# Performance work log

Hardware: AMD Instinct MI355X
Metric: run time of the kernel (lower is better)

Reference implementation:

```python
import jax, jax.numpy as jnp
import numpy as np

B, N, D, A, H, DFF = 4, 2048, 1024, 1024, 16, 4096
HD = A // H
SCALE = D ** (-0.5)  # module uses d_model**-0.5, not head_dim
EPS = 1e-5


def setup_inputs() -> dict:
    key = jax.random.key(0)
    ks = jax.random.split(key, 16)
    s = lambda k, shp, fan: jax.random.normal(k, shp, jnp.float32) * (fan ** -0.5)
    return {
        "x": jax.random.normal(ks[0], (B, N, D), jnp.float32),
        "mask": jnp.zeros((B, 1, N, N), dtype=bool),
        "wq": s(ks[1], (A, D), D), "bq": jnp.zeros((A,), jnp.float32),
        "wk": s(ks[2], (A, D), D), "bk": jnp.zeros((A,), jnp.float32),
        "wv": s(ks[3], (A, D), D), "bv": jnp.zeros((A,), jnp.float32),
        "wo": s(ks[4], (D, A), A), "bo": jnp.zeros((D,), jnp.float32),
        "w1": s(ks[5], (DFF, D), D), "b1": jnp.zeros((DFF,), jnp.float32),
        "w2": s(ks[6], (D, DFF), DFF), "b2": jnp.zeros((D,), jnp.float32),
        "ln1_g": jnp.ones((D,), jnp.float32), "ln1_b": jnp.zeros((D,), jnp.float32),
        "ln2_g": jnp.ones((D,), jnp.float32), "ln2_b": jnp.zeros((D,), jnp.float32),
    }


def _ln(x, g, b):
    m = x.mean(-1, keepdims=True)
    v = jnp.mean((x - m) ** 2, -1, keepdims=True)
    return (x - m) * jax.lax.rsqrt(v + EPS) * g + b


def reference(x, mask, wq, bq, wk, bk, wv, bv, wo, bo, w1, b1, w2, b2,
              ln1_g, ln1_b, ln2_g, ln2_b):
    # --- pre-norm self attention ---
    h = _ln(x, ln1_g, ln1_b)
    def heads(w, bias):  # (B,N,D) -> (B,H,N,HD)
        y = h @ w.T + bias
        return y.reshape(B, N, H, HD).transpose(0, 2, 1, 3)
    q, k, v = heads(wq, bq), heads(wk, bk), heads(wv, bv)
    scores = jnp.einsum('bhnd,bhmd->bhnm', q, k) * SCALE
    scores = jnp.where(mask, -jnp.inf, scores)
    attn = jax.nn.softmax(scores, axis=-1)  # dropout = identity in eval
    o = jnp.einsum('bhnm,bhmd->bhnd', attn, v)
    o = o.transpose(0, 2, 1, 3).reshape(B, N, A)
    x = (o @ wo.T + bo) + x
    # --- pre-norm MLP ---
    h2 = _ln(x, ln2_g, ln2_b)
    m = jax.nn.relu(h2 @ w1.T + b1) @ w2.T + b2
    return m + x
```

## Files before the change

### kernel.cpp

```cpp
#include <hip/hip_runtime.h>
#include <hip/hip_bf16.h>
#include <stdint.h>

#define Bb 4
#define Nn 2048
#define Dd 1024
#define Aa 1024
#define Hh 16
#define HDd 64
#define DFF 4096
#define Mm (Bb*Nn)

typedef __bf16 bf16x8 __attribute__((ext_vector_type(8)));
typedef float f32x4 __attribute__((ext_vector_type(4)));
typedef float f32x16 __attribute__((ext_vector_type(16)));
typedef uint32_t u32x4v __attribute__((ext_vector_type(4)));
typedef unsigned short ushort_t;
using bf16 = __hip_bfloat16;

#define LOG2E 1.44269504088896340736f

__device__ inline ushort_t f2bfu(float f) {
  uint32_t u = __builtin_bit_cast(uint32_t, f);
  uint32_t r = u + 0x7fffu + ((u >> 16) & 1u);
  return (ushort_t)(r >> 16);
}
__device__ inline uint32_t pk2(float lo, float hi) {
  return ((uint32_t)f2bfu(hi) << 16) | (uint32_t)f2bfu(lo);
}

#define GLOAD_LDS16(gsrc, ldst)                                                \
  __builtin_amdgcn_global_load_lds(                                            \
      (const __attribute__((address_space(1))) void*)(gsrc),                   \
      (__attribute__((address_space(3))) void*)(ldst), 16, 0, 0)

__global__ __launch_bounds__(256) void cvt_k(const float* __restrict__ in,
                                             bf16* __restrict__ out, int n4) {
  int i = blockIdx.x * 256 + threadIdx.x;
  if (i >= n4) return;
  float4 v = reinterpret_cast<const float4*>(in)[i];
  ushort4 o;
  o.x = f2bfu(v.x); o.y = f2bfu(v.y); o.z = f2bfu(v.z); o.w = f2bfu(v.w);
  reinterpret_cast<ushort4*>(out)[i] = o;
}

__global__ __launch_bounds__(256) void ln_k(const float* __restrict__ x,
                                            const float* __restrict__ g,
                                            const float* __restrict__ b,
                                            bf16* __restrict__ out) {
  const int row = blockIdx.x;
  const int t = threadIdx.x;
  const float4 v = reinterpret_cast<const float4*>(x + (size_t)row * Dd)[t];
  float s = v.x + v.y + v.z + v.w;
  float sq = v.x * v.x + v.y * v.y + v.z * v.z + v.w * v.w;
#pragma unroll
  for (int m = 1; m < 64; m <<= 1) {
    s += __shfl_xor(s, m);
    sq += __shfl_xor(sq, m);
  }
  __shared__ float red[8];
  if ((t & 63) == 0) { red[t >> 6] = s; red[4 + (t >> 6)] = sq; }
  __syncthreads();
  s = red[0] + red[1] + red[2] + red[3];
  sq = red[4] + red[5] + red[6] + red[7];
  const float mean = s * (1.f / Dd);
  const float rstd = rsqrtf(sq * (1.f / Dd) - mean * mean + 1e-5f);
  const float4 gg = reinterpret_cast<const float4*>(g)[t];
  const float4 bb = reinterpret_cast<const float4*>(b)[t];
  ushort4 o;
  o.x = f2bfu((v.x - mean) * rstd * gg.x + bb.x);
  o.y = f2bfu((v.y - mean) * rstd * gg.y + bb.y);
  o.z = f2bfu((v.z - mean) * rstd * gg.z + bb.z);
  o.w = f2bfu((v.w - mean) * rstd * gg.w + bb.w);
  reinterpret_cast<ushort4*>(out + (size_t)row * Dd)[t] = o;
}

template <int EPI>
__global__ __launch_bounds__(256) void gemm_bt(const bf16* __restrict__ Amat,
                                               const bf16* __restrict__ Wmat,
                                               const float* __restrict__ bias,
                                               const float* __restrict__ resid,
                                               void* __restrict__ Cout,
                                               int Ndim, int Kdim, float ascale) {
  __shared__ __align__(16) bf16 As[128 * 32];
  __shared__ __align__(16) bf16 Bs[128 * 32];
  const int tid = threadIdx.x;
  const int wave = tid >> 6, lane = tid & 63;
  const int g16 = lane >> 4, l15 = lane & 15;
  const int wm = wave >> 1, wn = wave & 1;
  const int tmb = blockIdx.y * 128, tnb = blockIdx.x * 128;

  const f32x4 zero = {0.f, 0.f, 0.f, 0.f};
  f32x4 acc[4][4];
#pragma unroll
  for (int f = 0; f < 4; f++)
#pragma unroll
    for (int g = 0; g < 4; g++) acc[f][g] = zero;

  for (int k0 = 0; k0 < Kdim; k0 += 32) {
    __syncthreads();
#pragma unroll
    for (int i = 0; i < 2; i++) {
      int c = i * 256 + tid;
      int row = c >> 2, cw = c & 3;
      GLOAD_LDS16(Amat + (size_t)(tmb + row) * Kdim + k0 + cw * 8,
                  As + (i * 256 + wave * 64) * 8);
      GLOAD_LDS16(Wmat + (size_t)(tnb + row) * Kdim + k0 + cw * 8,
                  Bs + (i * 256 + wave * 64) * 8);
    }
    __syncthreads();
    bf16x8 af[4], bfr[4];
#pragma unroll
    for (int f = 0; f < 4; f++) {
      af[f] = *reinterpret_cast<const bf16x8*>(As + (wm * 64 + f * 16 + l15) * 32 + g16 * 8);
      bfr[f] = *reinterpret_cast<const bf16x8*>(Bs + (wn * 64 + f * 16 + l15) * 32 + g16 * 8);
    }
#pragma unroll
    for (int f = 0; f < 4; f++)
#pragma unroll
      for (int g = 0; g < 4; g++)
        acc[f][g] = __builtin_amdgcn_mfma_f32_16x16x32_bf16(af[f], bfr[g], acc[f][g], 0, 0, 0);
  }

#pragma unroll
  for (int f = 0; f < 4; f++) {
#pragma unroll
    for (int g = 0; g < 4; g++) {
      const int col = tnb + wn * 64 + g * 16 + l15;
      const float bi = bias[col];
#pragma unroll
      for (int r = 0; r < 4; r++) {
        const int row = tmb + wm * 64 + f * 16 + g16 * 4 + r;
        float v = (acc[f][g][r] + bi) * ascale;
        if constexpr (EPI == 2) v = fmaxf(v, 0.f);
        if constexpr (EPI == 1) {
          ((float*)Cout)[(size_t)row * Ndim + col] = v + resid[(size_t)row * Ndim + col];
        } else {
          ((bf16*)Cout)[(size_t)row * Ndim + col] = __float2bfloat16(v);
        }
      }
    }
  }
}

__global__ __launch_bounds__(256) void vtrans_k(const bf16* __restrict__ vm,
                                                bf16* __restrict__ vt) {
  const int bh = blockIdx.y, b = bh >> 4, h = bh & 15;
  const int n0 = blockIdx.x * 64;
  __shared__ __align__(16) bf16 tile[64 * 72];
  const int tid = threadIdx.x;
#pragma unroll
  for (int i = 0; i < 2; i++) {
    int c = i * 256 + tid;
    int r = c >> 3, cw = c & 7;
    bf16x8 v = *reinterpret_cast<const bf16x8*>(vm + (size_t)(b * Nn + n0 + r) * Aa + h * HDd + cw * 8);
    *reinterpret_cast<bf16x8*>(tile + r * 72 + cw * 8) = v;
  }
  __syncthreads();
#pragma unroll
  for (int i = 0; i < 2; i++) {
    int c = i * 256 + tid;
    int d = c >> 3, ncw = c & 7;
    alignas(16) bf16 tmp[8];
#pragma unroll
    for (int e = 0; e < 8; e++) tmp[e] = tile[(ncw * 8 + e) * 72 + d];
    *reinterpret_cast<bf16x8*>(vt + (size_t)(bh * HDd + d) * Nn + n0 + ncw * 8) =
        *reinterpret_cast<bf16x8*>(tmp);
  }
}

__global__ __launch_bounds__(256) void attn_k(const bf16* __restrict__ qm,
                                              const bf16* __restrict__ km,
                                              const bf16* __restrict__ vtm,
                                              bf16* __restrict__ om) {
  const int bh = blockIdx.y, b = bh >> 4, h = bh & 15;
  const int tid = threadIdx.x;
  const int wv = tid >> 6, lane = tid & 63;
  const int l31 = lane & 31, hi = lane >> 5, l7 = lane & 7;

  __shared__ __align__(16) bf16 SMEM[16384];

  const int q0 = blockIdx.x * 128 + wv * 32;

  bf16x8 qf[4];
  const size_t qbase = (size_t)(b * Nn + q0 + l31) * Aa + h * HDd + hi * 8;
#pragma unroll
  for (int dk = 0; dk < 4; dk++)
    qf[dk] = *reinterpret_cast<const bf16x8*>(qm + qbase + dk * 16);

  f32x16 oacc[2];
#pragma unroll
  for (int d = 0; d < 2; d++)
#pragma unroll
    for (int r = 0; r < 16; r++) oacc[d][r] = 0.f;
  float mrun = -__builtin_huge_valf(), lrun = 0.f;

#define STAGE(buf, j0)                                                         \
  {                                                                            \
    _Pragma("unroll")                                                          \
    for (int i = 0; i < 2; i++) {                                              \
      int id = i * 256 + tid;                                                  \
      int row = id >> 3, c = id & 7;                                           \
      int cs = c ^ (row & 7);                                                  \
      GLOAD_LDS16(km + (size_t)(b * Nn + (j0) + row) * Aa + h * HDd + cs * 8,  \
                  SMEM + (buf) * 4096 + (i * 256 + wv * 64) * 8);              \
      GLOAD_LDS16(vtm + (size_t)(bh * 64 + row) * Nn + (j0) + cs * 8,          \
                  SMEM + 8192 + (buf) * 4096 + (i * 256 + wv * 64) * 8);       \
    }                                                                          \
  }

  STAGE(0, 0)
  asm volatile("s_waitcnt vmcnt(0)" ::: "memory");
  __builtin_amdgcn_s_barrier();

  const int NT = Nn / 64;
  for (int jt = 0; jt < NT; jt++) {
    const int cur = jt & 1;
    if (jt + 1 < NT) STAGE(cur ^ 1, (jt + 1) * 64)
    const bf16* KBc = SMEM + cur * 4096;
    const bf16* VBc = SMEM + 8192 + cur * 4096;

    f32x16 sacc[2];
#pragma unroll
    for (int t = 0; t < 2; t++)
#pragma unroll
      for (int r = 0; r < 16; r++) sacc[t][r] = 0.f;
#pragma unroll
    for (int t = 0; t < 2; t++) {
#pragma unroll
      for (int dk = 0; dk < 4; dk++) {
        const int row = t * 32 + l31;
        const bf16x8 kf = *reinterpret_cast<const bf16x8*>(
            KBc + row * 64 + (((hi + 2 * dk) ^ l7) * 8));
        sacc[t] = __builtin_amdgcn_mfma_f32_32x32x16_bf16(kf, qf[dk], sacc[t], 0, 0, 0);
      }
    }

    float tm = sacc[0][0];
#pragma unroll
    for (int r = 1; r < 16; r++) tm = fmaxf(tm, sacc[0][r]);
#pragma unroll
    for (int r = 0; r < 16; r++) tm = fmaxf(tm, sacc[1][r]);
    tm = fmaxf(tm, __shfl_xor(tm, 32));
    const float nm = fmaxf(mrun, tm);
    const float corr = exp2f((mrun - nm) * LOG2E);
    mrun = nm;

    float ps = 0.f;
    uint32_t w[8][2];
#pragma unroll
    for (int a = 0; a < 8; a++) {
#pragma unroll
      for (int bb = 0; bb < 2; bb++) {
        const int t = a >> 2, r = (a & 3) * 4 + 2 * bb;
        const float p0 = exp2f((sacc[t][r] - nm) * LOG2E);
        const float p1 = exp2f((sacc[t][r + 1] - nm) * LOG2E);
        ps += p0 + p1;
        w[a][bb] = pk2(p0, p1);
      }
    }
    ps += __shfl_xor(ps, 32);
    lrun = lrun * corr + ps;
#pragma unroll
    for (int d = 0; d < 2; d++)
#pragma unroll
      for (int r = 0; r < 16; r++) oacc[d][r] *= corr;

#pragma unroll
    for (int ks = 0; ks < 4; ks++) {
      const uint32_t wl0 = hi ? w[2 * ks + 1][0] : w[2 * ks][0];
      const uint32_t wl1 = hi ? w[2 * ks + 1][1] : w[2 * ks][1];
      const uint32_t ws0 = hi ? w[2 * ks][0] : w[2 * ks + 1][0];
      const uint32_t ws1 = hi ? w[2 * ks][1] : w[2 * ks + 1][1];
      const uint32_t wr0 = __shfl_xor(ws0, 32);
      const uint32_t wr1 = __shfl_xor(ws1, 32);
      u32x4v w4;
      w4[0] = hi ? wr0 : wl0;
      w4[1] = hi ? wr1 : wl1;
      w4[2] = hi ? wl0 : wr0;
      w4[3] = hi ? wl1 : wr1;
      const bf16x8 pf = __builtin_bit_cast(bf16x8, w4);
#pragma unroll
      for (int dh = 0; dh < 2; dh++) {
        const int row = dh * 32 + l31;
        const bf16x8 vf = *reinterpret_cast<const bf16x8*>(
            VBc + row * 64 + (((hi + 2 * ks) ^ l7) * 8));
        oacc[dh] = __builtin_amdgcn_mfma_f32_32x32x16_bf16(vf, pf, oacc[dh], 0, 0, 0);
      }
    }

    if (jt + 1 < NT) {
      asm volatile("s_waitcnt vmcnt(0)" ::: "memory");
      __builtin_amdgcn_s_barrier();
    }
  }

  __syncthreads();
  bf16* ob = SMEM + wv * (32 * 72);
  const float inv = 1.f / lrun;
#pragma unroll
  for (int dh = 0; dh < 2; dh++) {
#pragma unroll
    for (int r = 0; r < 16; r++) {
      const int d = (r & 3) + 8 * (r >> 2) + 4 * hi + 32 * dh;
      ob[l31 * 72 + d] = __float2bfloat16(oacc[dh][r] * inv);
    }
  }
  __syncthreads();
  const int qp = lane >> 1, half = lane & 1;
  const size_t orow = (size_t)(b * Nn + q0 + qp) * Aa + h * HDd + half * 32;
#pragma unroll
  for (int e = 0; e < 2; e++) {
    bf16x8 v0 = *reinterpret_cast<const bf16x8*>(ob + qp * 72 + half * 32 + e * 16);
    bf16x8 v1 = *reinterpret_cast<const bf16x8*>(ob + qp * 72 + half * 32 + e * 16 + 8);
    *reinterpret_cast<bf16x8*>(om + orow + e * 16) = v0;
    *reinterpret_cast<bf16x8*>(om + orow + e * 16 + 8) = v1;
  }
}

extern "C" void kernel_launch(void* const* d_in, const int* in_sizes, int n_in,
                              void* d_out, int out_size, void* d_ws, size_t ws_size,
                              hipStream_t stream) {
  const float* x    = (const float*)d_in[0];
  const float* wq   = (const float*)d_in[2];
  const float* bq   = (const float*)d_in[3];
  const float* wk   = (const float*)d_in[4];
  const float* bk   = (const float*)d_in[5];
  const float* wv   = (const float*)d_in[6];
  const float* bv   = (const float*)d_in[7];
  const float* wo   = (const float*)d_in[8];
  const float* bo   = (const float*)d_in[9];
  const float* w1   = (const float*)d_in[10];
  const float* b1   = (const float*)d_in[11];
  const float* w2   = (const float*)d_in[12];
  const float* b2   = (const float*)d_in[13];
  const float* ln1g = (const float*)d_in[14];
  const float* ln1b = (const float*)d_in[15];
  const float* ln2g = (const float*)d_in[16];
  const float* ln2b = (const float*)d_in[17];
  float* out = (float*)d_out;

  uint8_t* ws = (uint8_t*)d_ws;
  const size_t MB = (size_t)1 << 20;
  bf16* wq_b = (bf16*)(ws + 0 * MB);
  bf16* wk_b = (bf16*)(ws + 2 * MB);
  bf16* wv_b = (bf16*)(ws + 4 * MB);
  bf16* wo_b = (bf16*)(ws + 6 * MB);
  bf16* w1_b = (bf16*)(ws + 8 * MB);
  bf16* w2_b = (bf16*)(ws + 16 * MB);
  bf16* h_b  = (bf16*)(ws + 24 * MB);
  bf16* q_b  = (bf16*)(ws + 40 * MB);
  bf16* k_b  = (bf16*)(ws + 56 * MB);
  bf16* v_b  = (bf16*)(ws + 72 * MB);
  bf16* vt_b = (bf16*)(ws + 88 * MB);
  bf16* o_b  = (bf16*)(ws + 104 * MB);
  float* x2  = (float*)(ws + 120 * MB);
  bf16* mid  = (bf16*)(ws + 40 * MB);

  const float SCALE = 0.03125f;

  cvt_k<<<1024, 256, 0, stream>>>(wq, wq_b, 262144);
  cvt_k<<<1024, 256, 0, stream>>>(wk, wk_b, 262144);
  cvt_k<<<1024, 256, 0, stream>>>(wv, wv_b, 262144);
  cvt_k<<<1024, 256, 0, stream>>>(wo, wo_b, 262144);
  cvt_k<<<4096, 256, 0, stream>>>(w1, w1_b, 1048576);
  cvt_k<<<4096, 256, 0, stream>>>(w2, w2_b, 1048576);

  ln_k<<<Mm, 256, 0, stream>>>(x, ln1g, ln1b, h_b);

  dim3 gP(Aa / 128, Mm / 128);
  gemm_bt<0><<<gP, 256, 0, stream>>>(h_b, wq_b, bq, nullptr, q_b, Aa, Dd, SCALE);
  gemm_bt<0><<<gP, 256, 0, stream>>>(h_b, wk_b, bk, nullptr, k_b, Aa, Dd, 1.f);
  gemm_bt<0><<<gP, 256, 0, stream>>>(h_b, wv_b, bv, nullptr, v_b, Aa, Dd, 1.f);

  vtrans_k<<<dim3(Nn / 64, Bb * Hh), 256, 0, stream>>>(v_b, vt_b);
  attn_k<<<dim3(Nn / 128, Bb * Hh), 256, 0, stream>>>(q_b, k_b, vt_b, o_b);

  gemm_bt<1><<<gP, 256, 0, stream>>>(o_b, wo_b, bo, x, x2, Dd, Aa, 1.f);

  ln_k<<<Mm, 256, 0, stream>>>(x2, ln2g, ln2b, h_b);

  dim3 gF(DFF / 128, Mm / 128);
  gemm_bt<2><<<gF, 256, 0, stream>>>(h_b, w1_b, b1, nullptr, mid, DFF, Dd, 1.f);
  gemm_bt<1><<<gP, 256, 0, stream>>>(mid, w2_b, b2, x2, out, Dd, DFF, 1.f);
}
```

Baseline: 692.5 us.

## Swizzle GEMM LDS layout, lazy softmax rescale, hardware bf16 pack, permlane swap

The GEMM tiles are now stored in LDS with an XOR-swizzled two-rows-per-64-element layout, so the MFMA fragment reads avoid bank conflicts. The attention kernel skips rescaling the output accumulator unless the running max grows by more than a threshold (lazy rescale). It also packs to bf16 with v_cvt_pk_bf16_f32, replaces the shuffle-based P fragment exchange with v_permlane32_swap, and splits the row-sum into independent partial sums. The attention grid is transposed so that heads vary fastest, which changes K/V cache locality. The lazy rescale lets unnormalized exponentials reach up to 2^(8*log2e) before normalization, which carries a small numeric risk.

After: 659.2 us. -4.8%, faster.

```diff
diff --git a/kernel.cpp b/kernel.cpp
--- a/kernel.cpp
+++ b/kernel.cpp
@@ -24,9 +24,6 @@
   uint32_t u = __builtin_bit_cast(uint32_t, f);
   uint32_t r = u + 0x7fffu + ((u >> 16) & 1u);
   return (ushort_t)(r >> 16);
-}
-__device__ inline uint32_t pk2(float lo, float hi) {
-  return ((uint32_t)f2bfu(hi) << 16) | (uint32_t)f2bfu(lo);
 }
 
 #define GLOAD_LDS16(gsrc, ldst)                                                \
@@ -101,19 +98,26 @@
     __syncthreads();
 #pragma unroll
     for (int i = 0; i < 2; i++) {
-      int c = i * 256 + tid;
-      int row = c >> 2, cw = c & 3;
-      GLOAD_LDS16(Amat + (size_t)(tmb + row) * Kdim + k0 + cw * 8,
+      int t = i * 256 + tid;
+      int lr = t >> 3;
+      int s8 = (t & 7) ^ (lr & 7);
+      int row = lr * 2 + (s8 >> 2);
+      int cs = s8 & 3;
+      GLOAD_LDS16(Amat + (size_t)(tmb + row) * Kdim + k0 + cs * 8,
                   As + (i * 256 + wave * 64) * 8);
-      GLOAD_LDS16(Wmat + (size_t)(tnb + row) * Kdim + k0 + cw * 8,
+      GLOAD_LDS16(Wmat + (size_t)(tnb + row) * Kdim + k0 + cs * 8,
                   Bs + (i * 256 + wave * 64) * 8);
     }
     __syncthreads();
     bf16x8 af[4], bfr[4];
 #pragma unroll
     for (int f = 0; f < 4; f++) {
-      af[f] = *reinterpret_cast<const bf16x8*>(As + (wm * 64 + f * 16 + l15) * 32 + g16 * 8);
-      bfr[f] = *reinterpret_cast<const bf16x8*>(Bs + (wn * 64 + f * 16 + l15) * 32 + g16 * 8);
+      const int rA = wm * 64 + f * 16 + l15;
+      const int rB = wn * 64 + f * 16 + l15;
+      af[f] = *reinterpret_cast<const bf16x8*>(
+          As + (rA >> 1) * 64 + (((((rA & 1) << 2) + g16) ^ ((rA >> 1) & 7)) * 8));
+      bfr[f] = *reinterpret_cast<const bf16x8*>(
+          Bs + (rB >> 1) * 64 + (((((rB & 1) << 2) + g16) ^ ((rB >> 1) & 7)) * 8));
     }
 #pragma unroll
     for (int f = 0; f < 4; f++)
@@ -173,14 +177,14 @@
                                               const bf16* __restrict__ km,
                                               const bf16* __restrict__ vtm,
                                               bf16* __restrict__ om) {
-  const int bh = blockIdx.y, b = bh >> 4, h = bh & 15;
+  const int bh = blockIdx.x, b = bh >> 4, h = bh & 15;
   const int tid = threadIdx.x;
   const int wv = tid >> 6, lane = tid & 63;
   const int l31 = lane & 31, hi = lane >> 5, l7 = lane & 7;
 
   __shared__ __align__(16) bf16 SMEM[16384];
 
-  const int q0 = blockIdx.x * 128 + wv * 32;
+  const int q0 = blockIdx.y * 128 + wv * 32;
 
   bf16x8 qf[4];
   const size_t qbase = (size_t)(b * Nn + q0 + l31) * Aa + h * HDd + hi * 8;
@@ -236,49 +240,52 @@
       }
     }
 
-    float tm = sacc[0][0];
-#pragma unroll
-    for (int r = 1; r < 16; r++) tm = fmaxf(tm, sacc[0][r]);
+    float tm = fmaxf(sacc[0][0], sacc[0][1]);
+#pragma unroll
+    for (int r = 2; r < 16; r++) tm = fmaxf(tm, sacc[0][r]);
 #pragma unroll
     for (int r = 0; r < 16; r++) tm = fmaxf(tm, sacc[1][r]);
     tm = fmaxf(tm, __shfl_xor(tm, 32));
-    const float nm = fmaxf(mrun, tm);
-    const float corr = exp2f((mrun - nm) * LOG2E);
-    mrun = nm;
-
-    float ps = 0.f;
-    uint32_t w[8][2];
-#pragma unroll
-    for (int a = 0; a < 8; a++) {
-#pragma unroll
-      for (int bb = 0; bb < 2; bb++) {
-        const int t = a >> 2, r = (a & 3) * 4 + 2 * bb;
-        const float p0 = exp2f((sacc[t][r] - nm) * LOG2E);
-        const float p1 = exp2f((sacc[t][r + 1] - nm) * LOG2E);
-        ps += p0 + p1;
-        w[a][bb] = pk2(p0, p1);
+
+    if (!__all(tm <= mrun + 8.f)) {
+      const float nmv = fmaxf(mrun, tm);
+      const float corr = exp2f((mrun - nmv) * LOG2E);
+      mrun = nmv;
+      lrun *= corr;
+#pragma unroll
+      for (int d = 0; d < 2; d++)
+#pragma unroll
+        for (int r = 0; r < 16; r++) oacc[d][r] *= corr;
+    }
+    const float nmL = mrun * LOG2E;
+    float ps0 = 0.f, ps1 = 0.f, ps2 = 0.f, ps3 = 0.f;
+    uint32_t Wx[2][8];
+#pragma unroll
+    for (int t = 0; t < 2; t++) {
+#pragma unroll
+      for (int j = 0; j < 8; j++) {
+        const float p0 = exp2f(fmaf(sacc[t][2 * j], LOG2E, -nmL));
+        const float p1 = exp2f(fmaf(sacc[t][2 * j + 1], LOG2E, -nmL));
+        if (j & 2) { if (j & 1) ps3 += p0 + p1; else ps2 += p0 + p1; }
+        else       { if (j & 1) ps1 += p0 + p1; else ps0 += p0 + p1; }
+        uint32_t w;
+        asm("v_cvt_pk_bf16_f32 %0, %1, %2" : "=v"(w) : "v"(p0), "v"(p1));
+        Wx[t][j] = w;
       }
     }
+    float ps = (ps0 + ps1) + (ps2 + ps3);
     ps += __shfl_xor(ps, 32);
-    lrun = lrun * corr + ps;
-#pragma unroll
-    for (int d = 0; d < 2; d++)
-#pragma unroll
-      for (int r = 0; r < 16; r++) oacc[d][r] *= corr;
+    lrun += ps;
 
 #pragma unroll
     for (int ks = 0; ks < 4; ks++) {
-      const uint32_t wl0 = hi ? w[2 * ks + 1][0] : w[2 * ks][0];
-      const uint32_t wl1 = hi ? w[2 * ks + 1][1] : w[2 * ks][1];
-      const uint32_t ws0 = hi ? w[2 * ks][0] : w[2 * ks + 1][0];
-      const uint32_t ws1 = hi ? w[2 * ks][1] : w[2 * ks + 1][1];
-      const uint32_t wr0 = __shfl_xor(ws0, 32);
-      const uint32_t wr1 = __shfl_xor(ws1, 32);
+      const int tt = ks >> 1, bse = (ks & 1) * 4;
+      uint32_t w0 = Wx[tt][bse + 0], w1 = Wx[tt][bse + 1];
+      uint32_t w2 = Wx[tt][bse + 2], w3 = Wx[tt][bse + 3];
+      asm("v_permlane32_swap_b32 %0, %1" : "+v"(w0), "+v"(w2));
+      asm("v_permlane32_swap_b32 %0, %1" : "+v"(w1), "+v"(w3));
       u32x4v w4;
-      w4[0] = hi ? wr0 : wl0;
-      w4[1] = hi ? wr1 : wl1;
-      w4[2] = hi ? wl0 : wr0;
-      w4[3] = hi ? wl1 : wr1;
+      w4[0] = w0; w4[1] = w1; w4[2] = w2; w4[3] = w3;
       const bf16x8 pf = __builtin_bit_cast(bf16x8, w4);
 #pragma unroll
       for (int dh = 0; dh < 2; dh++) {
@@ -374,7 +381,7 @@
   gemm_bt<0><<<gP, 256, 0, stream>>>(h_b, wv_b, bv, nullptr, v_b, Aa, Dd, 1.f);
 
   vtrans_k<<<dim3(Nn / 64, Bb * Hh), 256, 0, stream>>>(v_b, vt_b);
-  attn_k<<<dim3(Nn / 128, Bb * Hh), 256, 0, stream>>>(q_b, k_b, vt_b, o_b);
+  attn_k<<<dim3(Bb * Hh, Nn / 128), 256, 0, stream>>>(q_b, k_b, vt_b, o_b);
 
   gemm_bt<1><<<gP, 256, 0, stream>>>(o_b, wo_b, bo, x, x2, Dd, Aa, 1.f);
 
```
